# Kernel optimization log

Measured on AMD Instinct MI355X. Metric: run time of the kernel, lower is better.

## Reference

```python
import jax, jax.numpy as jnp
import numpy as np

KERNEL_SIZE = 4  # kernel_size=4, dim=1, degree-1 open B-splines (SplineConv defaults)


def spline_conv(x, edge_index, edge_attr, W, root, bias):
    """SplineConv with dim=1, kernel_size=4, degree=1, open splines, aggr='mean'.

    x: [N, F_in]; edge_index: [2, E] (row 0 = source, row 1 = target);
    edge_attr: [E, 1] pseudo-coords in [0,1]; W: [K, F_in, F_out];
    root: [F_in, F_out]; bias: [F_out].
    """
    N = x.shape[0]
    src, dst = edge_index[0], edge_index[1]
    u = edge_attr[:, 0]                          # [E]
    v = u * (KERNEL_SIZE - 1)                    # open spline: scale by K-1
    vf = jnp.floor(v)
    frac = v - vf                                # [E], degree-1 basis fraction
    k0 = jnp.clip(vf.astype(jnp.int32), 0, KERNEL_SIZE - 1)
    k1 = jnp.minimum(k0 + 1, KERNEL_SIZE - 1)
    # Project node features through all K kernel weights once: [N, K, F_out]
    xw = jnp.einsum('nf,kfo->nko', x, W)
    # Per-edge message: basis-weighted mix of the two active kernel projections
    m = (1.0 - frac)[:, None] * xw[src, k0] + frac[:, None] * xw[src, k1]  # [E, F_out]
    # Mean aggregation at target nodes
    agg = jax.ops.segment_sum(m, dst, num_segments=N)               # [N, F_out]
    deg = jax.ops.segment_sum(jnp.ones_like(u), dst, num_segments=N)
    agg = agg / jnp.maximum(deg, 1.0)[:, None]
    return agg + x @ root + bias


def setup_inputs() -> dict:
    key = jax.random.key(0)
    ks = jax.random.split(key, 9)
    N, E, F_IN, HID, C = 50000, 1600000, 48, 32, 10
    x = jax.random.normal(ks[0], (N, F_IN), dtype=jnp.float32)
    edge_index = jax.random.randint(ks[1], (2, E), 0, N, dtype=jnp.int64)
    edge_attr = jax.random.uniform(ks[2], (E, 1), dtype=jnp.float32)
    s = 0.1
    W1 = jax.random.normal(ks[3], (KERNEL_SIZE, F_IN, HID), dtype=jnp.float32) * s
    root1 = jax.random.normal(ks[4], (F_IN, HID), dtype=jnp.float32) * s
    bias1 = jax.random.normal(ks[5], (HID,), dtype=jnp.float32) * s
    W2 = jax.random.normal(ks[6], (KERNEL_SIZE, HID, C), dtype=jnp.float32) * s
    root2 = jax.random.normal(ks[7], (HID, C), dtype=jnp.float32) * s
    bias2 = jax.random.normal(ks[8], (C,), dtype=jnp.float32) * s
    return {"x": x, "edge_index": edge_index, "edge_attr": edge_attr,
            "W1": W1, "root1": root1, "bias1": bias1,
            "W2": W2, "root2": root2, "bias2": bias2}


def reference(x, edge_index, edge_attr, W1, root1, bias1, W2, root2, bias2):
    # dropout is identity in eval mode (training=self.training)
    h = spline_conv(x, edge_index, edge_attr, W1, root1, bias1)
    h = jax.nn.elu(h)
    h = spline_conv(h, edge_index, edge_attr, W2, root2, bias2)
    return jax.nn.log_softmax(h, axis=1)
```

## Files before the change

### kernel.cpp

```cpp
#include <hip/hip_runtime.h>
#include <math.h>


#define F_IN   48
#define HID    32
#define NCLS   10
#define KS     4
#define BKT_SH 8
#define TILE   4096

__device__ inline unsigned short f2bf(float f) {
    unsigned x = __float_as_uint(f);
    unsigned r = x + 0x7FFFu + ((x >> 16) & 1u);
    return (unsigned short)(r >> 16);
}
__device__ inline float bf2f(unsigned short u) {
    return __uint_as_float(((unsigned)u) << 16);
}


__global__ void bucket_hist_kernel(const int* __restrict__ ei, int* __restrict__ bcnt,
                                   int E, int NB) {
    __shared__ int lcnt[256];
    int t = threadIdx.x;
    lcnt[t] = 0;
    __syncthreads();
    int e0 = blockIdx.x * TILE;
    int n = min(TILE, E - e0);
    for (int r = 0; r < TILE / 256; ++r) {
        int i = r * 256 + t;
        if (i < n) atomicAdd(&lcnt[ei[E + e0 + i] >> BKT_SH], 1);
    }
    __syncthreads();
    if (t < NB && lcnt[t] > 0) atomicAdd(&bcnt[t], lcnt[t]);
}

__global__ void mini_scan_kernel(const int* __restrict__ bcnt, int* __restrict__ bbase,
                                 int* __restrict__ gcur, int NB) {
    __shared__ int a[256], c[256];
    int t = threadIdx.x;
    int v = (t < NB) ? bcnt[t] : 0;
    a[t] = v; c[t] = v;
    __syncthreads();
    for (int o = 1; o < 256; o <<= 1) {
        int w = (t >= o) ? a[t - o] : 0;
        __syncthreads();
        a[t] += w;
        __syncthreads();
    }
    int ex = a[t] - c[t];
    if (t < NB) { bbase[t] = ex; gcur[t] = ex; }
    if (t == 0) bbase[NB] = a[255];
}

__global__ void bucket_scatter_kernel(const int* __restrict__ ei, const float* __restrict__ ea,
                                      int* __restrict__ gcur, uint2* __restrict__ tpd,
                                      int E, int NB) {
    __shared__ unsigned spl[TILE];
    __shared__ unsigned short sdst[TILE];
    __shared__ unsigned short inv[TILE];
    __shared__ int lcnt[256], loff[256], lrank[256], gb[256];
    int t = threadIdx.x;
    lcnt[t] = 0; lrank[t] = 0;
    __syncthreads();
    int e0 = blockIdx.x * TILE;
    int n = min(TILE, E - e0);
    for (int r = 0; r < TILE / 256; ++r) {
        int i = r * 256 + t;
        if (i < n) {
            int e = e0 + i;
            int src = ei[e];
            int dst = ei[E + e];
            float u = ea[e];
            float v = u * (float)(KS - 1);
            float vf = floorf(v);
            int k0 = min(max((int)vf, 0), KS - 1);
            unsigned qf = (unsigned)((v - vf) * 16383.f + 0.5f);
            spl[i] = (unsigned)src | ((unsigned)k0 << 16) | (qf << 18);
            sdst[i] = (unsigned short)dst;
            atomicAdd(&lcnt[dst >> BKT_SH], 1);
        }
    }
    __syncthreads();
    loff[t] = lcnt[t];
    __syncthreads();
    for (int o = 1; o < 256; o <<= 1) {
        int w = (t >= o) ? loff[t - o] : 0;
        __syncthreads();
        loff[t] += w;
        __syncthreads();
    }
    int ex = loff[t] - lcnt[t];
    __syncthreads();
    loff[t] = ex;
    if (t < NB) gb[t] = atomicAdd(&gcur[t], lcnt[t]);
    __syncthreads();
    for (int r = 0; r < TILE / 256; ++r) {
        int i = r * 256 + t;
        if (i < n) {
            int b = sdst[i] >> BKT_SH;
            int p = loff[b] + atomicAdd(&lrank[b], 1);
            inv[p] = (unsigned short)i;
        }
    }
    __syncthreads();
    for (int r = 0; r < TILE / 256; ++r) {
        int j = r * 256 + t;
        if (j < n) {
            int i = inv[j];
            int d = sdst[i];
            int b = d >> BKT_SH;
            int pos = gb[b] + (j - loff[b]);
            tpd[pos] = make_uint2(spl[i], (unsigned)d);
        }
    }
}


__global__ __launch_bounds__(256) void nsort_xw1_kernel(
        const uint2* __restrict__ tpd, const int* __restrict__ bbase,
        unsigned* __restrict__ spk, int* __restrict__ offs, int N, int NB,
        const float* __restrict__ X, const float* __restrict__ W,
        const float* __restrict__ R, unsigned short* __restrict__ outk,
        float* __restrict__ outr) {
    __shared__ union {
        struct { int hc[256]; int hs[256]; int hr[256]; } ns;
        float lw[48 * 160];
    } sm;
    int t = threadIdx.x;
    if ((int)blockIdx.x < NB) {
        int b = blockIdx.x;
        int nb0 = b << BKT_SH;
        int nb = min(256, N - nb0);
        int base = bbase[b];
        int m = bbase[b + 1] - base;
        sm.ns.hc[t] = 0; sm.ns.hr[t] = 0;
        __syncthreads();
        for (int i = t; i < m; i += 256) atomicAdd(&sm.ns.hc[tpd[base + i].y - nb0], 1);
        __syncthreads();
        sm.ns.hs[t] = sm.ns.hc[t];
        __syncthreads();
        for (int o = 1; o < 256; o <<= 1) {
            int w = (t >= o) ? sm.ns.hs[t - o] : 0;
            __syncthreads();
            sm.ns.hs[t] += w;
            __syncthreads();
        }
        if (t < nb) offs[nb0 + t] = base + (sm.ns.hs[t] - sm.ns.hc[t]);
        if (b == NB - 1 && t == 0) offs[N] = base + m;
        for (int i = t; i < m; i += 256) {
            uint2 rec = tpd[base + i];
            int d = rec.y - nb0;
            int p = (sm.ns.hs[d] - sm.ns.hc[d]) + atomicAdd(&sm.ns.hr[d], 1);
            spk[base + p] = rec.x;
        }
        return;
    }
    int bx = blockIdx.x - NB;
    for (int i = t; i < 48 * 160; i += 256) {
        int f = i / 160;
        int col = i - f * 160;
        sm.lw[i] = (col < 128) ? W[(size_t)(col >> 5) * (48 * 32) + f * 32 + (col & 31)]
                               : R[f * 32 + (col - 128)];
    }
    __syncthreads();
    int g = t % 40;
    int lp = t / 40;
    if (lp >= 6) return;
    int n0 = (bx * 6 + lp) * 2;
    if (n0 + 1 >= N) return;
    const float4* X0 = (const float4*)(X + (size_t)n0 * F_IN);
    const float4* X1 = (const float4*)(X + (size_t)(n0 + 1) * F_IN);
    float4 x0[12], x1[12];
#pragma unroll
    for (int i = 0; i < 12; ++i) { x0[i] = X0[i]; x1[i] = X1[i]; }
    const float4* lw4 = (const float4*)sm.lw;
    float4 a0 = {0,0,0,0}, a1 = {0,0,0,0};
#pragma unroll
    for (int fb = 0; fb < 12; ++fb) {
        float4 v0 = x0[fb], v1 = x1[fb];
#pragma unroll
        for (int j = 0; j < 4; ++j) {
            float s0 = (j == 0) ? v0.x : (j == 1) ? v0.y : (j == 2) ? v0.z : v0.w;
            float s1 = (j == 0) ? v1.x : (j == 1) ? v1.y : (j == 2) ? v1.z : v1.w;
            float4 w = lw4[(fb * 4 + j) * 40 + g];
            a0.x = fmaf(s0, w.x, a0.x); a0.y = fmaf(s0, w.y, a0.y);
            a0.z = fmaf(s0, w.z, a0.z); a0.w = fmaf(s0, w.w, a0.w);
            a1.x = fmaf(s1, w.x, a1.x); a1.y = fmaf(s1, w.y, a1.y);
            a1.z = fmaf(s1, w.z, a1.z); a1.w = fmaf(s1, w.w, a1.w);
        }
    }
    if (g < 32) {
        uint2 u0, u1;
        u0.x = f2bf(a0.x) | ((unsigned)f2bf(a0.y) << 16);
        u0.y = f2bf(a0.z) | ((unsigned)f2bf(a0.w) << 16);
        u1.x = f2bf(a1.x) | ((unsigned)f2bf(a1.y) << 16);
        u1.y = f2bf(a1.z) | ((unsigned)f2bf(a1.w) << 16);
        *(uint2*)(outk + (size_t)n0 * (KS * HID) + g * 4) = u0;
        *(uint2*)(outk + (size_t)(n0 + 1) * (KS * HID) + g * 4) = u1;
    } else {
        int o = 4 * g - 128;
        *(float4*)(outr + (size_t)n0 * HID + o) = a0;
        *(float4*)(outr + (size_t)(n0 + 1) * HID + o) = a1;
    }
}

__global__ void xw2_kernel(const float* __restrict__ H, const float* __restrict__ W,
                           const float* __restrict__ R, unsigned short* __restrict__ outk,
                           float* __restrict__ outr, int n) {
    __shared__ float lw2[32 * 50];
    int t = threadIdx.x;
    for (int i = t; i < 32 * 50; i += 256) {
        int f = i / 50;
        int col = i - f * 50;
        lw2[i] = (col < 40) ? W[(size_t)(col / 10) * (32 * 10) + f * 10 + (col % 10)]
                            : R[f * 10 + (col - 40)];
    }
    __syncthreads();
    int total = (n / 2) * 25;
    int id = blockIdx.x * blockDim.x + t;
    if (id >= total) return;
    int p = id % 25;
    int pr = id / 25;
    int n0 = 2 * pr;
    const float4* H0 = (const float4*)(H + (size_t)n0 * HID);
    const float4* H1 = (const float4*)(H + (size_t)(n0 + 1) * HID);
    float4 h0[8], h1[8];
#pragma unroll
    for (int i = 0; i < 8; ++i) { h0[i] = H0[i]; h1[i] = H1[i]; }
    const float2* lwp = (const float2*)lw2;
    float ax0 = 0.f, ay0 = 0.f, ax1 = 0.f, ay1 = 0.f;
#pragma unroll
    for (int fb = 0; fb < 8; ++fb) {
        float4 v0 = h0[fb], v1 = h1[fb];
#pragma unroll
        for (int j = 0; j < 4; ++j) {
            float s0 = (j == 0) ? v0.x : (j == 1) ? v0.y : (j == 2) ? v0.z : v0.w;
            float s1 = (j == 0) ? v1.x : (j == 1) ? v1.y : (j == 2) ? v1.z : v1.w;
            float2 w = lwp[(fb * 4 + j) * 25 + p];
            ax0 = fmaf(s0, w.x, ax0); ay0 = fmaf(s0, w.y, ay0);
            ax1 = fmaf(s1, w.x, ax1); ay1 = fmaf(s1, w.y, ay1);
        }
    }
    int col = 2 * p;
    if (col < KS * NCLS) {
        *(unsigned*)(outk + (size_t)n0 * (KS * NCLS) + col) =
            f2bf(ax0) | ((unsigned)f2bf(ay0) << 16);
        *(unsigned*)(outk + (size_t)(n0 + 1) * (KS * NCLS) + col) =
            f2bf(ax1) | ((unsigned)f2bf(ay1) << 16);
    } else {
        int o = col - KS * NCLS;
        *(float2*)(outr + (size_t)n0 * NCLS + o) = make_float2(ax0, ay0);
        *(float2*)(outr + (size_t)(n0 + 1) * NCLS + o) = make_float2(ax1, ay1);
    }
}


#define DECODE32(p, row, dk, fr)                                          \
    {   int src_ = (p) & 0xFFFF;                                          \
        int k0_ = ((p) >> 16) & 3;                                        \
        int k1_ = min(k0_ + 1, KS - 1);                                   \
        fr = (float)((p) >> 18) * (1.f / 16383.f);                        \
        row = xwk + (size_t)src_ * (KS * HID) + k0_ * HID + cg * 4;       \
        dk = (k1_ - k0_) * HID; }

__device__ inline void fma4(uint2 v0, uint2 v1, float fr, float4& a) {
    float w0 = 1.f - fr;
    a.x = fmaf(w0, __uint_as_float(v0.x << 16), a.x);
    a.x = fmaf(fr, __uint_as_float(v1.x << 16), a.x);
    a.y = fmaf(w0, __uint_as_float(v0.x & 0xFFFF0000u), a.y);
    a.y = fmaf(fr, __uint_as_float(v1.x & 0xFFFF0000u), a.y);
    a.z = fmaf(w0, __uint_as_float(v0.y << 16), a.z);
    a.z = fmaf(fr, __uint_as_float(v1.y << 16), a.z);
    a.w = fmaf(w0, __uint_as_float(v0.y & 0xFFFF0000u), a.w);
    a.w = fmaf(fr, __uint_as_float(v1.y & 0xFFFF0000u), a.w);
}

__global__ void agg1_kernel(const unsigned short* __restrict__ xwk,
                            const float* __restrict__ xroot,
                            const int* __restrict__ offs, const unsigned* __restrict__ spk,
                            const float* __restrict__ bias, float* __restrict__ h, int n) {
    int lane = threadIdx.x & 63;
    int cg = lane & 7;
    int slot = lane >> 3;
    int node = blockIdx.x * 4 + (threadIdx.x >> 6);
    if (node >= n) return;
    int beg = offs[node];
    int end = offs[node + 1];
    float4 a0 = {0, 0, 0, 0}, a1 = {0, 0, 0, 0};
    int e = beg + slot;
    while (e + 24 < end) {
        unsigned p0 = spk[e], p1 = spk[e + 8], p2 = spk[e + 16], p3 = spk[e + 24];
        const unsigned short *r0, *r1, *r2, *r3;
        int d0, d1, d2, d3;
        float f0, f1, f2, f3;
        DECODE32(p0, r0, d0, f0);
        DECODE32(p1, r1, d1, f1);
        DECODE32(p2, r2, d2, f2);
        DECODE32(p3, r3, d3, f3);
        uint2 v00 = *(const uint2*)r0, v01 = *(const uint2*)(r0 + d0);
        uint2 v10 = *(const uint2*)r1, v11 = *(const uint2*)(r1 + d1);
        uint2 v20 = *(const uint2*)r2, v21 = *(const uint2*)(r2 + d2);
        uint2 v30 = *(const uint2*)r3, v31 = *(const uint2*)(r3 + d3);
        fma4(v00, v01, f0, a0);
        fma4(v10, v11, f1, a1);
        fma4(v20, v21, f2, a0);
        fma4(v30, v31, f3, a1);
        e += 32;
    }
    while (e < end) {
        unsigned p = spk[e];
        const unsigned short* r;
        int d;
        float f;
        DECODE32(p, r, d, f);
        uint2 v0 = *(const uint2*)r, v1 = *(const uint2*)(r + d);
        fma4(v0, v1, f, a0);
        e += 8;
    }
    float4 s;
    s.x = a0.x + a1.x; s.y = a0.y + a1.y; s.z = a0.z + a1.z; s.w = a0.w + a1.w;
#pragma unroll
    for (int m = 8; m < 64; m <<= 1) {
        s.x += __shfl_xor(s.x, m, 64);
        s.y += __shfl_xor(s.y, m, 64);
        s.z += __shfl_xor(s.z, m, 64);
        s.w += __shfl_xor(s.w, m, 64);
    }
    if (slot == 0) {
        int deg = end - beg;
        float inv = 1.f / (float)(deg > 0 ? deg : 1);
        float4 r = *(const float4*)(xroot + (size_t)node * HID + cg * 4);
        float4 b = *(const float4*)(bias + cg * 4);
        float4 o;
        o.x = fmaf(s.x, inv, r.x + b.x);
        o.y = fmaf(s.y, inv, r.y + b.y);
        o.z = fmaf(s.z, inv, r.z + b.z);
        o.w = fmaf(s.w, inv, r.w + b.w);
        o.x = (o.x > 0.f) ? o.x : expm1f(o.x);
        o.y = (o.y > 0.f) ? o.y : expm1f(o.y);
        o.z = (o.z > 0.f) ? o.z : expm1f(o.z);
        o.w = (o.w > 0.f) ? o.w : expm1f(o.w);
        *(float4*)(h + (size_t)node * HID + cg * 4) = o;
    }
}

__global__ void agg2_kernel(const unsigned short* __restrict__ xwk,
                            const float* __restrict__ xroot,
                            const int* __restrict__ offs, const unsigned* __restrict__ spk,
                            const float* __restrict__ bias, float* __restrict__ out, int n) {
    int lane = threadIdx.x & 63;
    int u = lane & 7;
    int slot = lane >> 3;
    int node = blockIdx.x * 4 + (threadIdx.x >> 6);
    bool nv = node < n;
    if (!nv) node = n - 1;
    int up = min(u, 4);
    int beg = offs[node];
    int end = offs[node + 1];
    float a0l = 0.f, a0h = 0.f, a1l = 0.f, a1h = 0.f;

#define DEC2(p, q0, q1, fr)                                               \
    {   int src_ = (p) & 0xFFFF;                                          \
        int k0_ = ((p) >> 16) & 3;                                        \
        int k1_ = min(k0_ + 1, KS - 1);                                   \
        fr = (float)((p) >> 18) * (1.f / 16383.f);                        \
        const unsigned short* row_ = xwk + (size_t)src_ * 40;             \
        q0 = (const unsigned*)(row_ + k0_ * 10) + up;                     \
        q1 = (const unsigned*)(row_ + k1_ * 10) + up; }

#define FMA2(t0, t1, fr, al, ah)                                          \
    {   float w0_ = 1.f - fr;                                             \
        al = fmaf(w0_, __uint_as_float((t0) << 16), al);                  \
        al = fmaf(fr,  __uint_as_float((t1) << 16), al);                  \
        ah = fmaf(w0_, __uint_as_float((t0) & 0xFFFF0000u), ah);          \
        ah = fmaf(fr,  __uint_as_float((t1) & 0xFFFF0000u), ah); }

    int e = beg + slot;
    while (e + 24 < end) {
        unsigned p0 = spk[e], p1 = spk[e + 8], p2 = spk[e + 16], p3 = spk[e + 24];
        const unsigned *q00, *q01, *q10, *q11, *q20, *q21, *q30, *q31;
        float f0, f1, f2, f3;
        DEC2(p0, q00, q01, f0);
        DEC2(p1, q10, q11, f1);
        DEC2(p2, q20, q21, f2);
        DEC2(p3, q30, q31, f3);
        unsigned t00 = *q00, t01 = *q01;
        unsigned t10 = *q10, t11 = *q11;
        unsigned t20 = *q20, t21 = *q21;
        unsigned t30 = *q30, t31 = *q31;
        FMA2(t00, t01, f0, a0l, a0h);
        FMA2(t10, t11, f1, a1l, a1h);
        FMA2(t20, t21, f2, a0l, a0h);
        FMA2(t30, t31, f3, a1l, a1h);
        e += 32;
    }
    while (e < end) {
        unsigned p = spk[e];
        const unsigned *q0, *q1;
        float f;
        DEC2(p, q0, q1, f);
        unsigned t0 = *q0, t1 = *q1;
        FMA2(t0, t1, f, a0l, a0h);
        e += 8;
    }
    float vl = a0l + a1l, vh = a0h + a1h;
    if (u > 4) { vl = 0.f; vh = 0.f; }
#pragma unroll
    for (int m = 8; m < 64; m <<= 1) {
        vl += __shfl_xor(vl, m, 64);
        vh += __shfl_xor(vh, m, 64);
    }
    int deg = end - beg;
    float invd = 1.f / (float)(deg > 0 ? deg : 1);
    float l0 = -INFINITY, l1 = -INFINITY;
    if (u < 5) {
        float2 xr = *(const float2*)(xroot + (size_t)node * NCLS + 2 * u);
        l0 = fmaf(vl, invd, xr.x + bias[2 * u]);
        l1 = fmaf(vh, invd, xr.y + bias[2 * u + 1]);
    }
    float mx = fmaxf(l0, l1);
#pragma unroll
    for (int m = 1; m < 8; m <<= 1) mx = fmaxf(mx, __shfl_xor(mx, m, 64));
    float sden = (u < 5) ? (expf(l0 - mx) + expf(l1 - mx)) : 0.f;
#pragma unroll
    for (int m = 1; m < 8; m <<= 1) sden += __shfl_xor(sden, m, 64);
    if (nv && slot == 0 && u < 5) {
        float ls = logf(sden);
        *(float2*)(out + (size_t)node * NCLS + 2 * u) =
            make_float2(l0 - mx - ls, l1 - mx - ls);
    }
}

extern "C" void kernel_launch(void* const* d_in, const int* in_sizes, int n_in,
                              void* d_out, int out_size, void* d_ws, size_t ws_size,
                              hipStream_t stream) {
    const float* x       = (const float*)d_in[0];
    const int*   ei      = (const int*)d_in[1];
    const float* ea      = (const float*)d_in[2];
    const float* W1      = (const float*)d_in[3];
    const float* root1   = (const float*)d_in[4];
    const float* bias1   = (const float*)d_in[5];
    const float* W2      = (const float*)d_in[6];
    const float* root2   = (const float*)d_in[7];
    const float* bias2   = (const float*)d_in[8];
    float* out = (float*)d_out;

    const int N = in_sizes[0] / F_IN;
    const int E = in_sizes[2];
    const int NB = (N + 255) >> BKT_SH;

    char* base = (char*)d_ws;
    size_t off = 0;
    auto alloc = [&](size_t bytes) {
        char* p = base + off;
        off = (off + bytes + 255) & ~(size_t)255;
        return (void*)p;
    };
    unsigned short* xwk1 = (unsigned short*)alloc((size_t)N * KS * HID * 2);
    float* xr1           = (float*)alloc((size_t)N * HID * 4);
    float* h             = (float*)alloc((size_t)N * HID * 4);
    int* offs            = (int*)alloc(((size_t)N + 1) * 4);
    int* bcnt            = (int*)alloc((size_t)NB * 4);
    int* bbase           = (int*)alloc(((size_t)NB + 1) * 4);
    int* gcur            = (int*)alloc((size_t)NB * 4);
    unsigned* spk        = (unsigned*)alloc((size_t)E * 4);
    uint2* tpd           = (uint2*)alloc((size_t)E * 8);
    unsigned short* xwk2 = xwk1;
    float* xr2           = xr1;
    if (ws_size < off) return;

    int ebk = (E + TILE - 1) / TILE;
    int xb  = (N + 11) / 12;

    hipMemsetAsync(bcnt, 0, (size_t)NB * 4, stream);
    bucket_hist_kernel<<<ebk, 256, 0, stream>>>(ei, bcnt, E, NB);
    mini_scan_kernel<<<1, 256, 0, stream>>>(bcnt, bbase, gcur, NB);
    bucket_scatter_kernel<<<ebk, 256, 0, stream>>>(ei, ea, gcur, tpd, E, NB);
    nsort_xw1_kernel<<<NB + xb, 256, 0, stream>>>(tpd, bbase, spk, offs, N, NB,
                                                  x, W1, root1, xwk1, xr1);
    agg1_kernel<<<(N + 3) / 4, 256, 0, stream>>>(xwk1, xr1, offs, spk, bias1, h, N);
    {
        int total = (N / 2) * 25;
        xw2_kernel<<<(total + 255) / 256, 256, 0, stream>>>(h, W2, root2, xwk2, xr2, N);
    }
    agg2_kernel<<<(N + 3) / 4, 256, 0, stream>>>(xwk2, xr2, offs, spk, bias2, out, N);
}
```

Baseline: 231.7 us.

## Build CSR via per-node degree atomics and scan instead of in-bucket node sort

Counts per-node in-degree with global atomics during the bucket histogram, then computes CSR offsets with a three-stage block scan that is fused into the existing scan and bucket-scatter launches. The per-bucket shared-memory node sort is replaced by a flat scatter that claims each edge's slot with a global atomicAdd on a per-node cursor, streaming tpd in original bucketed order. This removes the per-bucket histogram and scan pass, but adds 1.6M global atomics for degree, another 1.6M for slot claims, and one more kernel launch. Edge order within each node's list becomes nondeterministic.

```diff
diff --git a/kernel.cpp b/kernel.cpp
--- a/kernel.cpp
+++ b/kernel.cpp
@@ -20,7 +20,7 @@
 
 
 __global__ void bucket_hist_kernel(const int* __restrict__ ei, int* __restrict__ bcnt,
-                                   int E, int NB) {
+                                   int* __restrict__ deg, int E, int NB) {
     __shared__ int lcnt[256];
     int t = threadIdx.x;
     lcnt[t] = 0;
@@ -29,18 +29,52 @@
     int n = min(TILE, E - e0);
     for (int r = 0; r < TILE / 256; ++r) {
         int i = r * 256 + t;
-        if (i < n) atomicAdd(&lcnt[ei[E + e0 + i] >> BKT_SH], 1);
+        if (i < n) {
+            int d = ei[E + e0 + i];
+            atomicAdd(&lcnt[d >> BKT_SH], 1);
+            atomicAdd(&deg[d], 1);
+        }
     }
     __syncthreads();
     if (t < NB && lcnt[t] > 0) atomicAdd(&bcnt[t], lcnt[t]);
 }
 
-__global__ void mini_scan_kernel(const int* __restrict__ bcnt, int* __restrict__ bbase,
-                                 int* __restrict__ gcur, int NB) {
+__global__ void miniscan_scana_kernel(const int* __restrict__ bcnt, int* __restrict__ bbase,
+                                      int* __restrict__ gcur, int NB,
+                                      const int* __restrict__ deg, int* __restrict__ bsum,
+                                      int N) {
     __shared__ int a[256], c[256];
     int t = threadIdx.x;
-    int v = (t < NB) ? bcnt[t] : 0;
-    a[t] = v; c[t] = v;
+    if (blockIdx.x == 0) {
+        int v = (t < NB) ? bcnt[t] : 0;
+        a[t] = v; c[t] = v;
+        __syncthreads();
+        for (int o = 1; o < 256; o <<= 1) {
+            int w = (t >= o) ? a[t - o] : 0;
+            __syncthreads();
+            a[t] += w;
+            __syncthreads();
+        }
+        int ex = a[t] - c[t];
+        if (t < NB) { bbase[t] = ex; gcur[t] = ex; }
+        if (t == 0) bbase[NB] = a[255];
+        return;
+    }
+    int blk = blockIdx.x - 1;
+    int i = blk * 256 + t;
+    int v = (i < N) ? deg[i] : 0;
+#pragma unroll
+    for (int m = 1; m < 64; m <<= 1) v += __shfl_xor(v, m, 64);
+    if ((t & 63) == 0) c[t >> 6] = v;
+    __syncthreads();
+    if (t == 0) bsum[blk] = c[0] + c[1] + c[2] + c[3];
+}
+
+__global__ void scan_b_kernel(const int* __restrict__ bsum, int* __restrict__ bbase2, int nb) {
+    __shared__ int a[256];
+    int t = threadIdx.x;
+    int v = (t < nb) ? bsum[t] : 0;
+    a[t] = v;
     __syncthreads();
     for (int o = 1; o < 256; o <<= 1) {
         int w = (t >= o) ? a[t - o] : 0;
@@ -48,22 +82,43 @@
         a[t] += w;
         __syncthreads();
     }
-    int ex = a[t] - c[t];
-    if (t < NB) { bbase[t] = ex; gcur[t] = ex; }
-    if (t == 0) bbase[NB] = a[255];
-}
-
-__global__ void bucket_scatter_kernel(const int* __restrict__ ei, const float* __restrict__ ea,
-                                      int* __restrict__ gcur, uint2* __restrict__ tpd,
-                                      int E, int NB) {
-    __shared__ unsigned spl[TILE];
-    __shared__ unsigned short sdst[TILE];
-    __shared__ unsigned short inv[TILE];
-    __shared__ int lcnt[256], loff[256], lrank[256], gb[256];
+    if (t < nb) bbase2[t] = a[t] - v;
+}
+
+__global__ __launch_bounds__(256) void scanc_bscatter_kernel(
+        const int* __restrict__ deg, const int* __restrict__ bbase2,
+        int* __restrict__ offs, int* __restrict__ cur, int N, int E, int SCB,
+        const int* __restrict__ ei, const float* __restrict__ ea,
+        int* __restrict__ gcur, uint2* __restrict__ tpd, int NB) {
+    __shared__ union {
+        int a[256];
+        struct {
+            unsigned spl[TILE];
+            unsigned short sdst[TILE];
+            unsigned short inv[TILE];
+            int lcnt[256], loff[256], lrank[256], gb[256];
+        } bs;
+    } sm;
     int t = threadIdx.x;
-    lcnt[t] = 0; lrank[t] = 0;
-    __syncthreads();
-    int e0 = blockIdx.x * TILE;
+    if ((int)blockIdx.x < SCB) {
+        int i = blockIdx.x * 256 + t;
+        int v = (i < N) ? deg[i] : 0;
+        sm.a[t] = v;
+        __syncthreads();
+        for (int o = 1; o < 256; o <<= 1) {
+            int w = (t >= o) ? sm.a[t - o] : 0;
+            __syncthreads();
+            sm.a[t] += w;
+            __syncthreads();
+        }
+        int ex = bbase2[blockIdx.x] + sm.a[t] - v;
+        if (i < N) { offs[i] = ex; cur[i] = ex; }
+        if (i == N - 1) offs[N] = E;
+        return;
+    }
+    sm.bs.lcnt[t] = 0; sm.bs.lrank[t] = 0;
+    __syncthreads();
+    int e0 = (blockIdx.x - SCB) * TILE;
     int n = min(TILE, E - e0);
     for (int r = 0; r < TILE / 256; ++r) {
         int i = r * 256 + t;
@@ -76,92 +131,77 @@
             float vf = floorf(v);
             int k0 = min(max((int)vf, 0), KS - 1);
             unsigned qf = (unsigned)((v - vf) * 16383.f + 0.5f);
-            spl[i] = (unsigned)src | ((unsigned)k0 << 16) | (qf << 18);
-            sdst[i] = (unsigned short)dst;
-            atomicAdd(&lcnt[dst >> BKT_SH], 1);
-        }
-    }
-    __syncthreads();
-    loff[t] = lcnt[t];
+            sm.bs.spl[i] = (unsigned)src | ((unsigned)k0 << 16) | (qf << 18);
+            sm.bs.sdst[i] = (unsigned short)dst;
+            atomicAdd(&sm.bs.lcnt[dst >> BKT_SH], 1);
+        }
+    }
+    __syncthreads();
+    sm.bs.loff[t] = sm.bs.lcnt[t];
     __syncthreads();
     for (int o = 1; o < 256; o <<= 1) {
-        int w = (t >= o) ? loff[t - o] : 0;
+        int w = (t >= o) ? sm.bs.loff[t - o] : 0;
         __syncthreads();
-        loff[t] += w;
+        sm.bs.loff[t] += w;
         __syncthreads();
     }
-    int ex = loff[t] - lcnt[t];
-    __syncthreads();
-    loff[t] = ex;
-    if (t < NB) gb[t] = atomicAdd(&gcur[t], lcnt[t]);
+    int ex = sm.bs.loff[t] - sm.bs.lcnt[t];
+    __syncthreads();
+    sm.bs.loff[t] = ex;
+    if (t < NB) sm.bs.gb[t] = atomicAdd(&gcur[t], sm.bs.lcnt[t]);
     __syncthreads();
     for (int r = 0; r < TILE / 256; ++r) {
         int i = r * 256 + t;
         if (i < n) {
-            int b = sdst[i] >> BKT_SH;
-            int p = loff[b] + atomicAdd(&lrank[b], 1);
-            inv[p] = (unsigned short)i;
+            int b = sm.bs.sdst[i] >> BKT_SH;
+            int p = sm.bs.loff[b] + atomicAdd(&sm.bs.lrank[b], 1);
+            sm.bs.inv[p] = (unsigned short)i;
         }
     }
     __syncthreads();
     for (int r = 0; r < TILE / 256; ++r) {
         int j = r * 256 + t;
         if (j < n) {
-            int i = inv[j];
-            int d = sdst[i];
+            int i = sm.bs.inv[j];
+            int d = sm.bs.sdst[i];
             int b = d >> BKT_SH;
-            int pos = gb[b] + (j - loff[b]);
-            tpd[pos] = make_uint2(spl[i], (unsigned)d);
-        }
-    }
-}
-
-
-__global__ __launch_bounds__(256) void nsort_xw1_kernel(
-        const uint2* __restrict__ tpd, const int* __restrict__ bbase,
-        unsigned* __restrict__ spk, int* __restrict__ offs, int N, int NB,
+            int pos = sm.bs.gb[b] + (j - sm.bs.loff[b]);
+            tpd[pos] = make_uint2(sm.bs.spl[i], (unsigned)d);
+        }
+    }
+}
+
+
+#define SCAT_EPB 2048
+
+__global__ __launch_bounds__(256) void scatter_xw1_kernel(
+        const uint2* __restrict__ tpd, int* __restrict__ cur,
+        unsigned* __restrict__ spk, int E, int SB,
         const float* __restrict__ X, const float* __restrict__ W,
         const float* __restrict__ R, unsigned short* __restrict__ outk,
-        float* __restrict__ outr) {
-    __shared__ union {
-        struct { int hc[256]; int hs[256]; int hr[256]; } ns;
-        float lw[48 * 160];
-    } sm;
+        float* __restrict__ outr, int N) {
+    __shared__ float lw[48 * 160];
     int t = threadIdx.x;
-    if ((int)blockIdx.x < NB) {
-        int b = blockIdx.x;
-        int nb0 = b << BKT_SH;
-        int nb = min(256, N - nb0);
-        int base = bbase[b];
-        int m = bbase[b + 1] - base;
-        sm.ns.hc[t] = 0; sm.ns.hr[t] = 0;
-        __syncthreads();
-        for (int i = t; i < m; i += 256) atomicAdd(&sm.ns.hc[tpd[base + i].y - nb0], 1);
-        __syncthreads();
-        sm.ns.hs[t] = sm.ns.hc[t];
-        __syncthreads();
-        for (int o = 1; o < 256; o <<= 1) {
-            int w = (t >= o) ? sm.ns.hs[t - o] : 0;
-            __syncthreads();
-            sm.ns.hs[t] += w;
-            __syncthreads();
-        }
-        if (t < nb) offs[nb0 + t] = base + (sm.ns.hs[t] - sm.ns.hc[t]);
-        if (b == NB - 1 && t == 0) offs[N] = base + m;
-        for (int i = t; i < m; i += 256) {
-            uint2 rec = tpd[base + i];
-            int d = rec.y - nb0;
-            int p = (sm.ns.hs[d] - sm.ns.hc[d]) + atomicAdd(&sm.ns.hr[d], 1);
-            spk[base + p] = rec.x;
+    if ((int)blockIdx.x < SB) {
+        int e0 = blockIdx.x * SCAT_EPB;
+        int n = min(SCAT_EPB, E - e0);
+#pragma unroll
+        for (int r = 0; r < SCAT_EPB / 256; ++r) {
+            int i = r * 256 + t;
+            if (i < n) {
+                uint2 rec = tpd[e0 + i];
+                int pos = atomicAdd(&cur[rec.y], 1);
+                spk[pos] = rec.x;
+            }
         }
         return;
     }
-    int bx = blockIdx.x - NB;
+    int bx = blockIdx.x - SB;
     for (int i = t; i < 48 * 160; i += 256) {
         int f = i / 160;
         int col = i - f * 160;
-        sm.lw[i] = (col < 128) ? W[(size_t)(col >> 5) * (48 * 32) + f * 32 + (col & 31)]
-                               : R[f * 32 + (col - 128)];
+        lw[i] = (col < 128) ? W[(size_t)(col >> 5) * (48 * 32) + f * 32 + (col & 31)]
+                            : R[f * 32 + (col - 128)];
     }
     __syncthreads();
     int g = t % 40;
@@ -174,7 +214,7 @@
     float4 x0[12], x1[12];
 #pragma unroll
     for (int i = 0; i < 12; ++i) { x0[i] = X0[i]; x1[i] = X1[i]; }
-    const float4* lw4 = (const float4*)sm.lw;
+    const float4* lw4 = (const float4*)lw;
     float4 a0 = {0,0,0,0}, a1 = {0,0,0,0};
 #pragma unroll
     for (int fb = 0; fb < 12; ++fb) {
@@ -449,6 +489,7 @@
     const int N = in_sizes[0] / F_IN;
     const int E = in_sizes[2];
     const int NB = (N + 255) >> BKT_SH;
+    const int NBLK = (N + 255) >> 8;
 
     char* base = (char*)d_ws;
     size_t off = 0;
@@ -461,9 +502,14 @@
     float* xr1           = (float*)alloc((size_t)N * HID * 4);
     float* h             = (float*)alloc((size_t)N * HID * 4);
     int* offs            = (int*)alloc(((size_t)N + 1) * 4);
-    int* bcnt            = (int*)alloc((size_t)NB * 4);
+    int* zero0           = (int*)alloc(((size_t)N + 256) * 4);
+    int* deg             = zero0;
+    int* bcnt            = zero0 + N;
+    int* cur             = (int*)alloc((size_t)N * 4);
     int* bbase           = (int*)alloc(((size_t)NB + 1) * 4);
     int* gcur            = (int*)alloc((size_t)NB * 4);
+    int* bsum            = (int*)alloc((size_t)NBLK * 4);
+    int* bbase2          = (int*)alloc((size_t)NBLK * 4);
     unsigned* spk        = (unsigned*)alloc((size_t)E * 4);
     uint2* tpd           = (uint2*)alloc((size_t)E * 8);
     unsigned short* xwk2 = xwk1;
@@ -471,14 +517,19 @@
     if (ws_size < off) return;
 
     int ebk = (E + TILE - 1) / TILE;
+    int sb  = (E + SCAT_EPB - 1) / SCAT_EPB;
     int xb  = (N + 11) / 12;
 
-    hipMemsetAsync(bcnt, 0, (size_t)NB * 4, stream);
-    bucket_hist_kernel<<<ebk, 256, 0, stream>>>(ei, bcnt, E, NB);
-    mini_scan_kernel<<<1, 256, 0, stream>>>(bcnt, bbase, gcur, NB);
-    bucket_scatter_kernel<<<ebk, 256, 0, stream>>>(ei, ea, gcur, tpd, E, NB);
-    nsort_xw1_kernel<<<NB + xb, 256, 0, stream>>>(tpd, bbase, spk, offs, N, NB,
-                                                  x, W1, root1, xwk1, xr1);
+    hipMemsetAsync(zero0, 0, ((size_t)N + 256) * 4, stream);
+    bucket_hist_kernel<<<ebk, 256, 0, stream>>>(ei, bcnt, deg, E, NB);
+    miniscan_scana_kernel<<<1 + NBLK, 256, 0, stream>>>(bcnt, bbase, gcur, NB,
+                                                        deg, bsum, N);
+    scan_b_kernel<<<1, 256, 0, stream>>>(bsum, bbase2, NBLK);
+    scanc_bscatter_kernel<<<NBLK + ebk, 256, 0, stream>>>(deg, bbase2, offs, cur,
+                                                          N, E, NBLK,
+                                                          ei, ea, gcur, tpd, NB);
+    scatter_xw1_kernel<<<sb + xb, 256, 0, stream>>>(tpd, cur, spk, E, sb,
+                                                    x, W1, root1, xwk1, xr1, N);
     agg1_kernel<<<(N + 3) / 4, 256, 0, stream>>>(xwk1, xr1, offs, spk, bias1, h, N);
     {
         int total = (N / 2) * 25;
```

Result: slower. 313.9 us (+35.4%).
